# Kernel optimization log

Hardware: AMD Instinct MI355X
Metric: run time of the kernel (lower is better)

Reference implementation:

```python
import jax, jax.numpy as jnp
import numpy as np

TOP_K = 2

def setup_inputs() -> dict:
    key = jax.random.key(0)
    ks = jax.random.split(key, 7)
    B, L, D, H, E, S = 2, 2048, 1024, 512, 16, 2048
    s = lambda fan_in: (1.0 / np.sqrt(fan_in)).astype(np.float32)
    return {
        "x": jax.random.normal(ks[0], (B, L, D), jnp.float32),
        "gate_w": jax.random.normal(ks[1], (E, D), jnp.float32) * s(D),
        "w1": jax.random.normal(ks[2], (E, H, D), jnp.float32) * s(D),
        "w2": jax.random.normal(ks[3], (E, D, H), jnp.float32) * s(H),
        "sfc1": jax.random.normal(ks[4], (S, D), jnp.float32) * s(D),
        "sfc2": jax.random.normal(ks[5], (S, D), jnp.float32) * s(D),
        "sfc3": jax.random.normal(ks[6], (D, S), jnp.float32) * s(S),
    }

def reference(x, gate_w, w1, w2, sfc1, sfc2, sfc3):
    B, L, D = x.shape
    E = gate_w.shape[0]
    # shared expert: SwiGLU MLP
    shared = jnp.einsum("bls,ds->bld", jax.nn.silu(jnp.einsum("bld,sd->bls", x, sfc1)) * jnp.einsum("bld,sd->bls", x, sfc2), sfc3)
    # router: top-k over gate logits, softmax over selected logits only
    logits = jnp.einsum("bld,ed->ble", x, gate_w)
    top_w, top_idx = jax.lax.top_k(logits, TOP_K)           # [B,L,K]
    top_w = jax.nn.softmax(top_w, axis=-1)
    xf = x.reshape(-1, D)                                    # [T,D]
    T = xf.shape[0]
    idx = top_idx.reshape(T, TOP_K)
    wk = top_w.reshape(T, TOP_K)
    # dense combine weights [T,E]: routing weight where selected, else 0
    dispatch = jnp.zeros((T, E), xf.dtype).at[jnp.arange(T)[:, None], idx].add(wk)
    # all-expert dense compute, combined with dispatch weights (avoids [T,E,D])
    h = jax.nn.silu(jnp.einsum("td,ehd->teh", xf, w1))       # [T,E,H]
    moe = jnp.einsum("teh,te,edh->td", h, dispatch, w2)      # [T,D]
    return moe.reshape(B, L, D) + shared
```

## Files before the change

### kernel.cpp

```cpp
#include <hip/hip_runtime.h>
#include <stdint.h>

#define T_TOK 4096
#define D_DIM 1024
#define H_DIM 512
#define E_NUM 16
#define S_DIM 2048

#define DUAL_BLOCKS 512
#define MOE1_TILES_MAX 80
#define SHOUT_BLOCKS 256

typedef __attribute__((ext_vector_type(8))) __bf16 bf16x8;
typedef __attribute__((ext_vector_type(4))) float f32x4;

__device__ __forceinline__ uint16_t f2bf(float f) {
  uint32_t u = __float_as_uint(f);
  u += 0x7fffu + ((u >> 16) & 1u);
  return (uint16_t)(u >> 16);
}

__device__ __forceinline__ float bf2f(uint16_t u) {
  return __uint_as_float(((uint32_t)u) << 16);
}

__device__ __forceinline__ void gl_lds16(const void* g, void* l) {
  __builtin_amdgcn_global_load_lds(
      (const __attribute__((address_space(1))) void*)g,
      (__attribute__((address_space(3))) void*)l, 16, 0, 0);
}

__device__ __forceinline__ float silu_f(float v) {
  return v / (1.f + __expf(-v));
}

#define N4_X (T_TOK * D_DIM / 4)
#define N4_S (S_DIM * D_DIM / 4)
#define N4_W (E_NUM * H_DIM * D_DIM / 4)
#define N4_TOT (N4_X + 3 * N4_S + 2 * N4_W)

__global__ __launch_bounds__(256) void k_cast_all(
    const float* __restrict__ x, const float* __restrict__ sfc1,
    const float* __restrict__ sfc2, const float* __restrict__ sfc3,
    const float* __restrict__ w1, const float* __restrict__ w2,
    uint16_t* __restrict__ xb, uint16_t* __restrict__ s1b,
    uint16_t* __restrict__ s2b, uint16_t* __restrict__ s3b,
    uint16_t* __restrict__ w1b, uint16_t* __restrict__ w2b) {
  int i = blockIdx.x * 256 + threadIdx.x;
  if (i >= N4_TOT) return;
  const float* src; uint16_t* dst; int off;
  if (i < N4_X)                    { src = x;    dst = xb;  off = 0; }
  else if (i < N4_X + N4_S)        { src = sfc1; dst = s1b; off = N4_X; }
  else if (i < N4_X + 2 * N4_S)    { src = sfc2; dst = s2b; off = N4_X + N4_S; }
  else if (i < N4_X + 3 * N4_S)    { src = sfc3; dst = s3b; off = N4_X + 2 * N4_S; }
  else if (i < N4_X + 3 * N4_S + N4_W) { src = w1; dst = w1b; off = N4_X + 3 * N4_S; }
  else                             { src = w2;  dst = w2b; off = N4_X + 3 * N4_S + N4_W; }
  int j = i - off;
  float4 v = ((const float4*)src)[j];
  ushort4 o;
  o.x = f2bf(v.x); o.y = f2bf(v.y); o.z = f2bf(v.z); o.w = f2bf(v.w);
  ((ushort4*)dst)[j] = o;
}

__global__ void k_gwT(const float* __restrict__ gw, float4* __restrict__ gwT4) {
  int tid = blockIdx.x * 256 + threadIdx.x;
  if (tid >= E_NUM * (D_DIM / 4)) return;
  int k4 = tid & (D_DIM / 4 - 1);
  int e = tid >> 8;
  float4 v = ((const float4*)(gw + (size_t)e * D_DIM))[k4];
  gwT4[(size_t)k4 * E_NUM + e] = v;
}

__global__ __launch_bounds__(256) void k_router(
    const float* __restrict__ x, const float4* __restrict__ gwT4,
    int* __restrict__ top_idx, float* __restrict__ top_w) {
  const int wid = threadIdx.x >> 6, lane = threadIdx.x & 63;
  const int t = blockIdx.x * 4 + wid;
  const int e = lane & 15, q = lane >> 4;
  const float4* xr4 = (const float4*)(x + (size_t)t * D_DIM) + q * 64;
  const float4* g4 = gwT4 + (size_t)q * 64 * E_NUM + e;
  float acc = 0.f;
#pragma unroll 8
  for (int i = 0; i < 64; i++) {
    float4 xv = xr4[i];
    float4 gv = g4[(size_t)i * E_NUM];
    acc += xv.x * gv.x + xv.y * gv.y + xv.z * gv.z + xv.w * gv.w;
  }
  acc += __shfl_xor(acc, 16, 64);
  acc += __shfl_xor(acc, 32, 64);
  float v1 = acc; int i1 = e;
#pragma unroll
  for (int off = 1; off < 16; off <<= 1) {
    float ov = __shfl_xor(v1, off, 64);
    int oi = __shfl_xor(i1, off, 64);
    if (ov > v1 || (ov == v1 && oi < i1)) { v1 = ov; i1 = oi; }
  }
  float v2 = (e == i1) ? -1e30f : acc; int i2 = e;
#pragma unroll
  for (int off = 1; off < 16; off <<= 1) {
    float ov = __shfl_xor(v2, off, 64);
    int oi = __shfl_xor(i2, off, 64);
    if (ov > v2 || (ov == v2 && oi < i2)) { v2 = ov; i2 = oi; }
  }
  if (lane == 0) {
    float w0 = 1.f / (1.f + __expf(v2 - v1));
    top_idx[t * 2] = i1; top_idx[t * 2 + 1] = i2;
    top_w[t * 2] = w0;  top_w[t * 2 + 1] = 1.f - w0;
  }
}

__global__ __launch_bounds__(256) void k_hist(const int* __restrict__ top_idx,
                                              int* __restrict__ partial) {
  __shared__ int h[E_NUM];
  int tid = threadIdx.x;
  if (tid < E_NUM) h[tid] = 0;
  __syncthreads();
  int id = blockIdx.x * 256 + tid;
  atomicAdd(&h[top_idx[id]], 1);
  __syncthreads();
  if (tid < E_NUM) partial[blockIdx.x * E_NUM + tid] = h[tid];
}

__global__ void k_scan(const int* __restrict__ partial, int* __restrict__ bases,
                       int* __restrict__ offsets, int* __restrict__ tile_e,
                       int* __restrict__ tile_m, int* __restrict__ tile_cnt) {
  __shared__ int tot[E_NUM];
  int e = threadIdx.x;
  if (e < E_NUM) {
    int run = 0;
    for (int b = 0; b < 32; b++) { bases[b * E_NUM + e] = run; run += partial[b * E_NUM + e]; }
    tot[e] = run;
  }
  __syncthreads();
  if (e == 0) {
    int s = 0;
    for (int i = 0; i < E_NUM; i++) { offsets[i] = s; s += tot[i]; }
    offsets[E_NUM] = s;
    int cnt = 0;
    for (int i = 0; i < E_NUM; i++) {
      for (int m0 = 0; m0 < tot[i]; m0 += 128) {
        tile_e[cnt] = i; tile_m[cnt] = m0; cnt++;
      }
    }
    tile_cnt[0] = cnt;
  }
  __syncthreads();
  if (e < E_NUM) {
    int off = offsets[e];
    for (int b = 0; b < 32; b++) bases[b * E_NUM + e] += off;
  }
}

__global__ __launch_bounds__(256) void k_scatter(
    const int* __restrict__ top_idx, const float* __restrict__ top_w,
    const int* __restrict__ bases, int* __restrict__ slot_token,
    float* __restrict__ slot_w, int* __restrict__ slot_of) {
  __shared__ int cur[E_NUM];
  int tid = threadIdx.x;
  if (tid < E_NUM) cur[tid] = bases[blockIdx.x * E_NUM + tid];
  __syncthreads();
  int id = blockIdx.x * 256 + tid;
  int e = top_idx[id];
  int slot = atomicAdd(&cur[e], 1);
  slot_token[slot] = id >> 1;
  slot_w[slot] = top_w[id];
  slot_of[id] = slot;
}

__global__ __launch_bounds__(256) void k_stage1(
    const uint16_t* __restrict__ xb, const uint16_t* __restrict__ b1,
    const uint16_t* __restrict__ b2, uint16_t* __restrict__ hs,
    const uint16_t* __restrict__ w1b, const int* __restrict__ offsets,
    const int* __restrict__ slot_token, const int* __restrict__ tile_e,
    const int* __restrict__ tile_m, const int* __restrict__ tile_cnt,
    uint16_t* __restrict__ hbuf) {
  __shared__ uint16_t smem[3 * 4096];
  const int bid = blockIdx.x;
  const int tid = threadIdx.x, lane = tid & 63, wid = tid >> 6;
  const int wm = wid >> 1, wn = wid & 1;
  const int r = lane & 15, q = lane >> 4;
  const int row0 = tid >> 2, col8 = (tid & 3) * 8;

  if (bid < DUAL_BLOCKS) {
    const int bm0 = (bid & 31) * 128, bn0 = (bid >> 5) * 128;
    uint16_t* sA = smem; uint16_t* sB1 = smem + 4096; uint16_t* sB2 = smem + 8192;
    f32x4 acc1[4][4], acc2[4][4];
#pragma unroll
    for (int i = 0; i < 4; i++)
#pragma unroll
      for (int j = 0; j < 4; j++) {
        acc1[i][j] = (f32x4){0.f, 0.f, 0.f, 0.f};
        acc2[i][j] = (f32x4){0.f, 0.f, 0.f, 0.f};
      }
    const uint16_t* ga0 = xb + (size_t)(bm0 + row0) * D_DIM + col8;
    const uint16_t* ga1 = ga0 + 64 * D_DIM;
    const uint16_t* gb10 = b1 + (size_t)(bn0 + row0) * D_DIM + col8;
    const uint16_t* gb11 = gb10 + 64 * D_DIM;
    const uint16_t* gb20 = b2 + (size_t)(bn0 + row0) * D_DIM + col8;
    const uint16_t* gb21 = gb20 + 64 * D_DIM;
    for (int kt = 0; kt < D_DIM; kt += 32) {
      gl_lds16(ga0, sA + wid * 512);   gl_lds16(ga1, sA + 2048 + wid * 512);
      gl_lds16(gb10, sB1 + wid * 512); gl_lds16(gb11, sB1 + 2048 + wid * 512);
      gl_lds16(gb20, sB2 + wid * 512); gl_lds16(gb21, sB2 + 2048 + wid * 512);
      ga0 += 32; ga1 += 32; gb10 += 32; gb11 += 32; gb20 += 32; gb21 += 32;
      __syncthreads();
      bf16x8 a[4];
#pragma unroll
      for (int i = 0; i < 4; i++)
        a[i] = *(const bf16x8*)(sA + (wm * 64 + i * 16 + r) * 32 + q * 8);
#pragma unroll
      for (int j = 0; j < 4; j++) {
        bf16x8 b = *(const bf16x8*)(sB1 + (wn * 64 + j * 16 + r) * 32 + q * 8);
#pragma unroll
        for (int i = 0; i < 4; i++)
          acc1[i][j] = __builtin_amdgcn_mfma_f32_16x16x32_bf16(a[i], b, acc1[i][j], 0, 0, 0);
      }
#pragma unroll
      for (int j = 0; j < 4; j++) {
        bf16x8 b = *(const bf16x8*)(sB2 + (wn * 64 + j * 16 + r) * 32 + q * 8);
#pragma unroll
        for (int i = 0; i < 4; i++)
          acc2[i][j] = __builtin_amdgcn_mfma_f32_16x16x32_bf16(a[i], b, acc2[i][j], 0, 0, 0);
      }
      __syncthreads();
    }
#pragma unroll
    for (int i = 0; i < 4; i++)
#pragma unroll
      for (int j = 0; j < 4; j++)
#pragma unroll
        for (int rr = 0; rr < 4; rr++) {
          int row = bm0 + wm * 64 + i * 16 + q * 4 + rr;
          int col = bn0 + wn * 64 + j * 16 + r;
          hs[(size_t)row * S_DIM + col] = f2bf(silu_f(acc1[i][j][rr]) * acc2[i][j][rr]);
        }
  } else {
    int idx = bid - DUAL_BLOCKS;
    int t = idx >> 2;
    if (t >= tile_cnt[0]) return;
    const int n0 = (idx & 3) * 128;
    const int e = tile_e[t], m0 = tile_m[t];
    const int base = offsets[e];
    const int ne = offsets[e + 1] - base;
    uint16_t* sA = smem; uint16_t* sB = smem + 4096;
    f32x4 acc[4][4];
#pragma unroll
    for (int i = 0; i < 4; i++)
#pragma unroll
      for (int j = 0; j < 4; j++) acc[i][j] = (f32x4){0.f, 0.f, 0.f, 0.f};
    const int e0 = min(m0 + row0, ne - 1);
    const int e1 = min(m0 + row0 + 64, ne - 1);
    const uint16_t* ga0 = xb + (size_t)slot_token[base + e0] * D_DIM + col8;
    const uint16_t* ga1 = xb + (size_t)slot_token[base + e1] * D_DIM + col8;
    const uint16_t* wbase = w1b + (size_t)e * H_DIM * D_DIM;
    const uint16_t* gb0 = wbase + (size_t)(n0 + row0) * D_DIM + col8;
    const uint16_t* gb1 = gb0 + 64 * D_DIM;
    for (int kt = 0; kt < D_DIM; kt += 32) {
      gl_lds16(ga0, sA + wid * 512); gl_lds16(ga1, sA + 2048 + wid * 512);
      gl_lds16(gb0, sB + wid * 512); gl_lds16(gb1, sB + 2048 + wid * 512);
      ga0 += 32; ga1 += 32; gb0 += 32; gb1 += 32;
      __syncthreads();
      bf16x8 a[4], bb[4];
#pragma unroll
      for (int i = 0; i < 4; i++)
        a[i] = *(const bf16x8*)(sA + (wm * 64 + i * 16 + r) * 32 + q * 8);
#pragma unroll
      for (int j = 0; j < 4; j++)
        bb[j] = *(const bf16x8*)(sB + (wn * 64 + j * 16 + r) * 32 + q * 8);
#pragma unroll
      for (int i = 0; i < 4; i++)
#pragma unroll
        for (int j = 0; j < 4; j++)
          acc[i][j] = __builtin_amdgcn_mfma_f32_16x16x32_bf16(a[i], bb[j], acc[i][j], 0, 0, 0);
      __syncthreads();
    }
#pragma unroll
    for (int i = 0; i < 4; i++)
#pragma unroll
      for (int j = 0; j < 4; j++)
#pragma unroll
        for (int rr = 0; rr < 4; rr++) {
          int ent = m0 + wm * 64 + i * 16 + q * 4 + rr;
          if (ent < ne) {
            int col = n0 + wn * 64 + j * 16 + r;
            hbuf[(size_t)(base + ent) * H_DIM + col] = f2bf(silu_f(acc[i][j][rr]));
          }
        }
  }
}

__global__ __launch_bounds__(256) void k_stage2(
    const uint16_t* __restrict__ hsb, const uint16_t* __restrict__ sfc3b,
    float* __restrict__ out, const uint16_t* __restrict__ hbuf,
    const uint16_t* __restrict__ w2b, const int* __restrict__ offsets,
    const float* __restrict__ slot_w, const int* __restrict__ tile_e,
    const int* __restrict__ tile_m, const int* __restrict__ tile_cnt,
    uint16_t* __restrict__ slot_out) {
  __shared__ uint16_t smem[2 * 4096];
  const int bid = blockIdx.x;
  const int tid = threadIdx.x, lane = tid & 63, wid = tid >> 6;
  const int wm = wid >> 1, wn = wid & 1;
  const int r = lane & 15, q = lane >> 4;
  const int row0 = tid >> 2, col8 = (tid & 3) * 8;
  uint16_t* sA = smem; uint16_t* sB = smem + 4096;

  if (bid < SHOUT_BLOCKS) {
    const int bm0 = (bid & 31) * 128, bn0 = (bid >> 5) * 128;
    f32x4 acc[4][4];
#pragma unroll
    for (int i = 0; i < 4; i++)
#pragma unroll
      for (int j = 0; j < 4; j++) acc[i][j] = (f32x4){0.f, 0.f, 0.f, 0.f};
    const uint16_t* ga0 = hsb + (size_t)(bm0 + row0) * S_DIM + col8;
    const uint16_t* ga1 = ga0 + (size_t)64 * S_DIM;
    const uint16_t* gb0 = sfc3b + (size_t)(bn0 + row0) * S_DIM + col8;
    const uint16_t* gb1 = gb0 + (size_t)64 * S_DIM;
    for (int kt = 0; kt < S_DIM; kt += 32) {
      gl_lds16(ga0, sA + wid * 512); gl_lds16(ga1, sA + 2048 + wid * 512);
      gl_lds16(gb0, sB + wid * 512); gl_lds16(gb1, sB + 2048 + wid * 512);
      ga0 += 32; ga1 += 32; gb0 += 32; gb1 += 32;
      __syncthreads();
      bf16x8 a[4], bb[4];
#pragma unroll
      for (int i = 0; i < 4; i++)
        a[i] = *(const bf16x8*)(sA + (wm * 64 + i * 16 + r) * 32 + q * 8);
#pragma unroll
      for (int j = 0; j < 4; j++)
        bb[j] = *(const bf16x8*)(sB + (wn * 64 + j * 16 + r) * 32 + q * 8);
#pragma unroll
      for (int i = 0; i < 4; i++)
#pragma unroll
        for (int j = 0; j < 4; j++)
          acc[i][j] = __builtin_amdgcn_mfma_f32_16x16x32_bf16(a[i], bb[j], acc[i][j], 0, 0, 0);
      __syncthreads();
    }
#pragma unroll
    for (int i = 0; i < 4; i++)
#pragma unroll
      for (int j = 0; j < 4; j++)
#pragma unroll
        for (int rr = 0; rr < 4; rr++) {
          int row = bm0 + wm * 64 + i * 16 + q * 4 + rr;
          int col = bn0 + wn * 64 + j * 16 + r;
          out[(size_t)row * D_DIM + col] = acc[i][j][rr];
        }
  } else {
    int idx = bid - SHOUT_BLOCKS;
    int t = idx >> 3;
    if (t >= tile_cnt[0]) return;
    const int n0 = (idx & 7) * 128;
    const int e = tile_e[t], m0 = tile_m[t];
    const int base = offsets[e];
    const int ne = offsets[e + 1] - base;
    f32x4 acc[4][4];
#pragma unroll
    for (int i = 0; i < 4; i++)
#pragma unroll
      for (int j = 0; j < 4; j++) acc[i][j] = (f32x4){0.f, 0.f, 0.f, 0.f};
    const int e0 = min(m0 + row0, ne - 1);
    const int e1 = min(m0 + row0 + 64, ne - 1);
    const uint16_t* ga0 = hbuf + (size_t)(base + e0) * H_DIM + col8;
    const uint16_t* ga1 = hbuf + (size_t)(base + e1) * H_DIM + col8;
    const uint16_t* wbase = w2b + (size_t)e * D_DIM * H_DIM;
    const uint16_t* gb0 = wbase + (size_t)(n0 + row0) * H_DIM + col8;
    const uint16_t* gb1 = gb0 + 64 * H_DIM;
    for (int kt = 0; kt < H_DIM; kt += 32) {
      gl_lds16(ga0, sA + wid * 512); gl_lds16(ga1, sA + 2048 + wid * 512);
      gl_lds16(gb0, sB + wid * 512); gl_lds16(gb1, sB + 2048 + wid * 512);
      ga0 += 32; ga1 += 32; gb0 += 32; gb1 += 32;
      __syncthreads();
      bf16x8 a[4], bb[4];
#pragma unroll
      for (int i = 0; i < 4; i++)
        a[i] = *(const bf16x8*)(sA + (wm * 64 + i * 16 + r) * 32 + q * 8);
#pragma unroll
      for (int j = 0; j < 4; j++)
        bb[j] = *(const bf16x8*)(sB + (wn * 64 + j * 16 + r) * 32 + q * 8);
#pragma unroll
      for (int i = 0; i < 4; i++)
#pragma unroll
        for (int j = 0; j < 4; j++)
          acc[i][j] = __builtin_amdgcn_mfma_f32_16x16x32_bf16(a[i], bb[j], acc[i][j], 0, 0, 0);
      __syncthreads();
    }
#pragma unroll
    for (int i = 0; i < 4; i++) {
      int ent_base = m0 + wm * 64 + i * 16 + q * 4;
#pragma unroll
      for (int rr = 0; rr < 4; rr++) {
        int ent = ent_base + rr;
        if (ent < ne) {
          float w = slot_w[base + ent];
          uint16_t* orow = slot_out + (size_t)(base + ent) * D_DIM;
#pragma unroll
          for (int j = 0; j < 4; j++) {
            int col = n0 + wn * 64 + j * 16 + r;
            orow[col] = f2bf(w * acc[i][j][rr]);
          }
        }
      }
    }
  }
}

__global__ __launch_bounds__(256) void k_combine(
    const uint16_t* __restrict__ slot_out, const int* __restrict__ slot_of,
    float* __restrict__ out) {
  int t = blockIdx.x;
  int c = threadIdx.x;
  int s0 = slot_of[t * 2], s1 = slot_of[t * 2 + 1];
  ushort4 a = ((const ushort4*)(slot_out + (size_t)s0 * D_DIM))[c];
  ushort4 b = ((const ushort4*)(slot_out + (size_t)s1 * D_DIM))[c];
  float4* po = (float4*)(out + (size_t)t * D_DIM) + c;
  float4 o = *po;
  o.x += bf2f(a.x) + bf2f(b.x);
  o.y += bf2f(a.y) + bf2f(b.y);
  o.z += bf2f(a.z) + bf2f(b.z);
  o.w += bf2f(a.w) + bf2f(b.w);
  *po = o;
}

extern "C" void kernel_launch(void* const* d_in, const int* in_sizes, int n_in,
                              void* d_out, int out_size, void* d_ws, size_t ws_size,
                              hipStream_t stream) {
  const float* x     = (const float*)d_in[0];
  const float* gatew = (const float*)d_in[1];
  const float* w1    = (const float*)d_in[2];
  const float* w2    = (const float*)d_in[3];
  const float* sfc1  = (const float*)d_in[4];
  const float* sfc2  = (const float*)d_in[5];
  const float* sfc3  = (const float*)d_in[6];
  float* out = (float*)d_out;

  uint8_t* ws = (uint8_t*)d_ws;
  size_t off = 0;
  auto alloc = [&](size_t bytes) {
    void* p = ws + off;
    off = (off + bytes + 255) & ~(size_t)255;
    return p;
  };
  uint16_t* xb    = (uint16_t*)alloc((size_t)T_TOK * D_DIM * 2);
  uint16_t* sfc1b = (uint16_t*)alloc((size_t)S_DIM * D_DIM * 2);
  uint16_t* sfc2b = (uint16_t*)alloc((size_t)S_DIM * D_DIM * 2);
  uint16_t* sfc3b = (uint16_t*)alloc((size_t)D_DIM * S_DIM * 2);
  uint16_t* w1b   = (uint16_t*)alloc((size_t)E_NUM * H_DIM * D_DIM * 2);
  uint16_t* w2b   = (uint16_t*)alloc((size_t)E_NUM * D_DIM * H_DIM * 2);
  uint16_t* hsb   = (uint16_t*)alloc((size_t)T_TOK * S_DIM * 2);
  uint16_t* hbuf  = (uint16_t*)alloc((size_t)2 * T_TOK * H_DIM * 2);
  uint16_t* slot_out = (uint16_t*)alloc((size_t)2 * T_TOK * D_DIM * 2);
  float4* gwT4    = (float4*)alloc((size_t)D_DIM / 4 * E_NUM * 16);
  int*   top_idx  = (int*)alloc((size_t)T_TOK * 2 * 4);
  float* top_w    = (float*)alloc((size_t)T_TOK * 2 * 4);
  int*   partial  = (int*)alloc(32 * E_NUM * 4);
  int*   bases    = (int*)alloc(32 * E_NUM * 4);
  int*   offsets  = (int*)alloc((E_NUM + 1) * 4);
  int*   tile_e   = (int*)alloc(MOE1_TILES_MAX * 4);
  int*   tile_m   = (int*)alloc(MOE1_TILES_MAX * 4);
  int*   tile_cnt = (int*)alloc(4);
  int*   slot_token = (int*)alloc((size_t)2 * T_TOK * 4);
  float* slot_w   = (float*)alloc((size_t)2 * T_TOK * 4);
  int*   slot_of  = (int*)alloc((size_t)2 * T_TOK * 4);

  k_cast_all<<<(N4_TOT + 255) / 256, 256, 0, stream>>>(
      x, sfc1, sfc2, sfc3, w1, w2, xb, sfc1b, sfc2b, sfc3b, w1b, w2b);
  k_gwT<<<(E_NUM * D_DIM / 4 + 255) / 256, 256, 0, stream>>>(gatew, gwT4);
  k_router<<<T_TOK / 4, 256, 0, stream>>>(x, gwT4, top_idx, top_w);
  k_hist<<<32, 256, 0, stream>>>(top_idx, partial);
  k_scan<<<1, 64, 0, stream>>>(partial, bases, offsets, tile_e, tile_m, tile_cnt);
  k_scatter<<<32, 256, 0, stream>>>(top_idx, top_w, bases, slot_token, slot_w, slot_of);
  k_stage1<<<DUAL_BLOCKS + MOE1_TILES_MAX * 4, 256, 0, stream>>>(
      xb, sfc1b, sfc2b, hsb, w1b, offsets, slot_token, tile_e, tile_m, tile_cnt, hbuf);
  k_stage2<<<SHOUT_BLOCKS + MOE1_TILES_MAX * 8, 256, 0, stream>>>(
      hsb, sfc3b, out, hbuf, w2b, offsets, slot_w, tile_e, tile_m, tile_cnt, slot_out);
  k_combine<<<T_TOK, 256, 0, stream>>>(slot_out, slot_of, out);
}
```

Baseline: 349.5 us.

## Double-buffer LDS tiles with register prefetch in all GEMM loops

Replaces direct global-to-LDS loads with register-staged loads into a double-buffered LDS tile. The next K-slice is fetched into registers while the current slice's MFMAs run, then stored to the alternate buffer, leaving one barrier per iteration instead of two. This aims to hide global load latency behind compute. The cost is double the LDS footprint and extra VGPRs for the staged data, which may reduce occupancy.

```diff
diff --git a/kernel.cpp b/kernel.cpp
--- a/kernel.cpp
+++ b/kernel.cpp
@@ -22,12 +22,6 @@
 
 __device__ __forceinline__ float bf2f(uint16_t u) {
   return __uint_as_float(((uint32_t)u) << 16);
-}
-
-__device__ __forceinline__ void gl_lds16(const void* g, void* l) {
-  __builtin_amdgcn_global_load_lds(
-      (const __attribute__((address_space(1))) void*)g,
-      (__attribute__((address_space(3))) void*)l, 16, 0, 0);
 }
 
 __device__ __forceinline__ float silu_f(float v) {
@@ -167,6 +161,7 @@
   slot_of[id] = slot;
 }
 
+
 __global__ __launch_bounds__(256) void k_stage1(
     const uint16_t* __restrict__ xb, const uint16_t* __restrict__ b1,
     const uint16_t* __restrict__ b2, uint16_t* __restrict__ hs,
@@ -174,16 +169,19 @@
     const int* __restrict__ slot_token, const int* __restrict__ tile_e,
     const int* __restrict__ tile_m, const int* __restrict__ tile_cnt,
     uint16_t* __restrict__ hbuf) {
-  __shared__ uint16_t smem[3 * 4096];
+  __shared__ uint16_t smem[6 * 4096];
   const int bid = blockIdx.x;
   const int tid = threadIdx.x, lane = tid & 63, wid = tid >> 6;
   const int wm = wid >> 1, wn = wid & 1;
   const int r = lane & 15, q = lane >> 4;
   const int row0 = tid >> 2, col8 = (tid & 3) * 8;
+  const int st0 = tid * 8, st1 = 2048 + tid * 8;
 
   if (bid < DUAL_BLOCKS) {
     const int bm0 = (bid & 31) * 128, bn0 = (bid >> 5) * 128;
-    uint16_t* sA = smem; uint16_t* sB1 = smem + 4096; uint16_t* sB2 = smem + 8192;
+    uint16_t* sA = smem;
+    uint16_t* sB1 = smem + 8192;
+    uint16_t* sB2 = smem + 16384;
     f32x4 acc1[4][4], acc2[4][4];
 #pragma unroll
     for (int i = 0; i < 4; i++)
@@ -198,31 +196,75 @@
     const uint16_t* gb11 = gb10 + 64 * D_DIM;
     const uint16_t* gb20 = b2 + (size_t)(bn0 + row0) * D_DIM + col8;
     const uint16_t* gb21 = gb20 + 64 * D_DIM;
-    for (int kt = 0; kt < D_DIM; kt += 32) {
-      gl_lds16(ga0, sA + wid * 512);   gl_lds16(ga1, sA + 2048 + wid * 512);
-      gl_lds16(gb10, sB1 + wid * 512); gl_lds16(gb11, sB1 + 2048 + wid * 512);
-      gl_lds16(gb20, sB2 + wid * 512); gl_lds16(gb21, sB2 + 2048 + wid * 512);
+
+    uint4 pA0, pA1, pB10, pB11, pB20, pB21;
+    pA0 = *(const uint4*)ga0;   pA1 = *(const uint4*)ga1;
+    pB10 = *(const uint4*)gb10; pB11 = *(const uint4*)gb11;
+    pB20 = *(const uint4*)gb20; pB21 = *(const uint4*)gb21;
+    ga0 += 32; ga1 += 32; gb10 += 32; gb11 += 32; gb20 += 32; gb21 += 32;
+    *(uint4*)(sA + st0) = pA0;   *(uint4*)(sA + st1) = pA1;
+    *(uint4*)(sB1 + st0) = pB10; *(uint4*)(sB1 + st1) = pB11;
+    *(uint4*)(sB2 + st0) = pB20; *(uint4*)(sB2 + st1) = pB21;
+    __syncthreads();
+
+    int cur = 0;
+    for (int kt = 32; kt < D_DIM; kt += 32) {
+      pA0 = *(const uint4*)ga0;   pA1 = *(const uint4*)ga1;
+      pB10 = *(const uint4*)gb10; pB11 = *(const uint4*)gb11;
+      pB20 = *(const uint4*)gb20; pB21 = *(const uint4*)gb21;
       ga0 += 32; ga1 += 32; gb10 += 32; gb11 += 32; gb20 += 32; gb21 += 32;
+      {
+        const uint16_t* A = sA + cur * 4096;
+        const uint16_t* B1 = sB1 + cur * 4096;
+        const uint16_t* B2 = sB2 + cur * 4096;
+        bf16x8 a[4];
+#pragma unroll
+        for (int i = 0; i < 4; i++)
+          a[i] = *(const bf16x8*)(A + (wm * 64 + i * 16 + r) * 32 + q * 8);
+#pragma unroll
+        for (int j = 0; j < 4; j++) {
+          bf16x8 b = *(const bf16x8*)(B1 + (wn * 64 + j * 16 + r) * 32 + q * 8);
+#pragma unroll
+          for (int i = 0; i < 4; i++)
+            acc1[i][j] = __builtin_amdgcn_mfma_f32_16x16x32_bf16(a[i], b, acc1[i][j], 0, 0, 0);
+        }
+#pragma unroll
+        for (int j = 0; j < 4; j++) {
+          bf16x8 b = *(const bf16x8*)(B2 + (wn * 64 + j * 16 + r) * 32 + q * 8);
+#pragma unroll
+          for (int i = 0; i < 4; i++)
+            acc2[i][j] = __builtin_amdgcn_mfma_f32_16x16x32_bf16(a[i], b, acc2[i][j], 0, 0, 0);
+        }
+      }
+      int nxt = cur ^ 1;
+      *(uint4*)(sA + nxt * 4096 + st0) = pA0;   *(uint4*)(sA + nxt * 4096 + st1) = pA1;
+      *(uint4*)(sB1 + nxt * 4096 + st0) = pB10; *(uint4*)(sB1 + nxt * 4096 + st1) = pB11;
+      *(uint4*)(sB2 + nxt * 4096 + st0) = pB20; *(uint4*)(sB2 + nxt * 4096 + st1) = pB21;
       __syncthreads();
+      cur = nxt;
+    }
+    {
+      const uint16_t* A = sA + cur * 4096;
+      const uint16_t* B1 = sB1 + cur * 4096;
+      const uint16_t* B2 = sB2 + cur * 4096;
       bf16x8 a[4];
 #pragma unroll
       for (int i = 0; i < 4; i++)
-        a[i] = *(const bf16x8*)(sA + (wm * 64 + i * 16 + r) * 32 + q * 8);
+        a[i] = *(const bf16x8*)(A + (wm * 64 + i * 16 + r) * 32 + q * 8);
 #pragma unroll
       for (int j = 0; j < 4; j++) {
-        bf16x8 b = *(const bf16x8*)(sB1 + (wn * 64 + j * 16 + r) * 32 + q * 8);
+        bf16x8 b = *(const bf16x8*)(B1 + (wn * 64 + j * 16 + r) * 32 + q * 8);
 #pragma unroll
         for (int i = 0; i < 4; i++)
           acc1[i][j] = __builtin_amdgcn_mfma_f32_16x16x32_bf16(a[i], b, acc1[i][j], 0, 0, 0);
       }
 #pragma unroll
       for (int j = 0; j < 4; j++) {
-        bf16x8 b = *(const bf16x8*)(sB2 + (wn * 64 + j * 16 + r) * 32 + q * 8);
+        bf16x8 b = *(const bf16x8*)(B2 + (wn * 64 + j * 16 + r) * 32 + q * 8);
 #pragma unroll
         for (int i = 0; i < 4; i++)
           acc2[i][j] = __builtin_amdgcn_mfma_f32_16x16x32_bf16(a[i], b, acc2[i][j], 0, 0, 0);
       }
-      __syncthreads();
     }
 #pragma unroll
     for (int i = 0; i < 4; i++)
@@ -242,7 +284,8 @@
     const int e = tile_e[t], m0 = tile_m[t];
     const int base = offsets[e];
     const int ne = offsets[e + 1] - base;
-    uint16_t* sA = smem; uint16_t* sB = smem + 4096;
+    uint16_t* sA = smem;
+    uint16_t* sB = smem + 8192;
     f32x4 acc[4][4];
 #pragma unroll
     for (int i = 0; i < 4; i++)
@@ -255,24 +298,57 @@
     const uint16_t* wbase = w1b + (size_t)e * H_DIM * D_DIM;
     const uint16_t* gb0 = wbase + (size_t)(n0 + row0) * D_DIM + col8;
     const uint16_t* gb1 = gb0 + 64 * D_DIM;
-    for (int kt = 0; kt < D_DIM; kt += 32) {
-      gl_lds16(ga0, sA + wid * 512); gl_lds16(ga1, sA + 2048 + wid * 512);
-      gl_lds16(gb0, sB + wid * 512); gl_lds16(gb1, sB + 2048 + wid * 512);
+
+    uint4 pA0, pA1, pB0, pB1;
+    pA0 = *(const uint4*)ga0; pA1 = *(const uint4*)ga1;
+    pB0 = *(const uint4*)gb0; pB1 = *(const uint4*)gb1;
+    ga0 += 32; ga1 += 32; gb0 += 32; gb1 += 32;
+    *(uint4*)(sA + st0) = pA0; *(uint4*)(sA + st1) = pA1;
+    *(uint4*)(sB + st0) = pB0; *(uint4*)(sB + st1) = pB1;
+    __syncthreads();
+
+    int cur = 0;
+    for (int kt = 32; kt < D_DIM; kt += 32) {
+      pA0 = *(const uint4*)ga0; pA1 = *(const uint4*)ga1;
+      pB0 = *(const uint4*)gb0; pB1 = *(const uint4*)gb1;
       ga0 += 32; ga1 += 32; gb0 += 32; gb1 += 32;
+      {
+        const uint16_t* A = sA + cur * 4096;
+        const uint16_t* B = sB + cur * 4096;
+        bf16x8 a[4], bb[4];
+#pragma unroll
+        for (int i = 0; i < 4; i++)
+          a[i] = *(const bf16x8*)(A + (wm * 64 + i * 16 + r) * 32 + q * 8);
+#pragma unroll
+        for (int j = 0; j < 4; j++)
+          bb[j] = *(const bf16x8*)(B + (wn * 64 + j * 16 + r) * 32 + q * 8);
+#pragma unroll
+        for (int i = 0; i < 4; i++)
+#pragma unroll
+          for (int j = 0; j < 4; j++)
+            acc[i][j] = __builtin_amdgcn_mfma_f32_16x16x32_bf16(a[i], bb[j], acc[i][j], 0, 0, 0);
+      }
+      int nxt = cur ^ 1;
+      *(uint4*)(sA + nxt * 4096 + st0) = pA0; *(uint4*)(sA + nxt * 4096 + st1) = pA1;
+      *(uint4*)(sB + nxt * 4096 + st0) = pB0; *(uint4*)(sB + nxt * 4096 + st1) = pB1;
       __syncthreads();
+      cur = nxt;
+    }
+    {
+      const uint16_t* A = sA + cur * 4096;
+      const uint16_t* B = sB + cur * 4096;
       bf16x8 a[4], bb[4];
 #pragma unroll
       for (int i = 0; i < 4; i++)
-        a[i] = *(const bf16x8*)(sA + (wm * 64 + i * 16 + r) * 32 + q * 8);
+        a[i] = *(const bf16x8*)(A + (wm * 64 + i * 16 + r) * 32 + q * 8);
 #pragma unroll
       for (int j = 0; j < 4; j++)
-        bb[j] = *(const bf16x8*)(sB + (wn * 64 + j * 16 + r) * 32 + q * 8);
+        bb[j] = *(const bf16x8*)(B + (wn * 64 + j * 16 + r) * 32 + q * 8);
 #pragma unroll
       for (int i = 0; i < 4; i++)
 #pragma unroll
         for (int j = 0; j < 4; j++)
           acc[i][j] = __builtin_amdgcn_mfma_f32_16x16x32_bf16(a[i], bb[j], acc[i][j], 0, 0, 0);
-      __syncthreads();
     }
 #pragma unroll
     for (int i = 0; i < 4; i++)
@@ -296,13 +372,15 @@
     const float* __restrict__ slot_w, const int* __restrict__ tile_e,
     const int* __restrict__ tile_m, const int* __restrict__ tile_cnt,
     uint16_t* __restrict__ slot_out) {
-  __shared__ uint16_t smem[2 * 4096];
+  __shared__ uint16_t smem[4 * 4096];
   const int bid = blockIdx.x;
   const int tid = threadIdx.x, lane = tid & 63, wid = tid >> 6;
   const int wm = wid >> 1, wn = wid & 1;
   const int r = lane & 15, q = lane >> 4;
   const int row0 = tid >> 2, col8 = (tid & 3) * 8;
-  uint16_t* sA = smem; uint16_t* sB = smem + 4096;
+  const int st0 = tid * 8, st1 = 2048 + tid * 8;
+  uint16_t* sA = smem;
+  uint16_t* sB = smem + 8192;
 
   if (bid < SHOUT_BLOCKS) {
     const int bm0 = (bid & 31) * 128, bn0 = (bid >> 5) * 128;
@@ -315,24 +393,57 @@
     const uint16_t* ga1 = ga0 + (size_t)64 * S_DIM;
     const uint16_t* gb0 = sfc3b + (size_t)(bn0 + row0) * S_DIM + col8;
     const uint16_t* gb1 = gb0 + (size_t)64 * S_DIM;
-    for (int kt = 0; kt < S_DIM; kt += 32) {
-      gl_lds16(ga0, sA + wid * 512); gl_lds16(ga1, sA + 2048 + wid * 512);
-      gl_lds16(gb0, sB + wid * 512); gl_lds16(gb1, sB + 2048 + wid * 512);
+
+    uint4 pA0, pA1, pB0, pB1;
+    pA0 = *(const uint4*)ga0; pA1 = *(const uint4*)ga1;
+    pB0 = *(const uint4*)gb0; pB1 = *(const uint4*)gb1;
+    ga0 += 32; ga1 += 32; gb0 += 32; gb1 += 32;
+    *(uint4*)(sA + st0) = pA0; *(uint4*)(sA + st1) = pA1;
+    *(uint4*)(sB + st0) = pB0; *(uint4*)(sB + st1) = pB1;
+    __syncthreads();
+
+    int cur = 0;
+    for (int kt = 32; kt < S_DIM; kt += 32) {
+      pA0 = *(const uint4*)ga0; pA1 = *(const uint4*)ga1;
+      pB0 = *(const uint4*)gb0; pB1 = *(const uint4*)gb1;
       ga0 += 32; ga1 += 32; gb0 += 32; gb1 += 32;
+      {
+        const uint16_t* A = sA + cur * 4096;
+        const uint16_t* B = sB + cur * 4096;
+        bf16x8 a[4], bb[4];
+#pragma unroll
+        for (int i = 0; i < 4; i++)
+          a[i] = *(const bf16x8*)(A + (wm * 64 + i * 16 + r) * 32 + q * 8);
+#pragma unroll
+        for (int j = 0; j < 4; j++)
+          bb[j] = *(const bf16x8*)(B + (wn * 64 + j * 16 + r) * 32 + q * 8);
+#pragma unroll
+        for (int i = 0; i < 4; i++)
+#pragma unroll
+          for (int j = 0; j < 4; j++)
+            acc[i][j] = __builtin_amdgcn_mfma_f32_16x16x32_bf16(a[i], bb[j], acc[i][j], 0, 0, 0);
+      }
+      int nxt = cur ^ 1;
+      *(uint4*)(sA + nxt * 4096 + st0) = pA0; *(uint4*)(sA + nxt * 4096 + st1) = pA1;
+      *(uint4*)(sB + nxt * 4096 + st0) = pB0; *(uint4*)(sB + nxt * 4096 + st1) = pB1;
       __syncthreads();
+      cur = nxt;
+    }
+    {
+      const uint16_t* A = sA + cur * 4096;
+      const uint16_t* B = sB + cur * 4096;
       bf16x8 a[4], bb[4];
 #pragma unroll
       for (int i = 0; i < 4; i++)
-        a[i] = *(const bf16x8*)(sA + (wm * 64 + i * 16 + r) * 32 + q * 8);
+        a[i] = *(const bf16x8*)(A + (wm * 64 + i * 16 + r) * 32 + q * 8);
 #pragma unroll
       for (int j = 0; j < 4; j++)
-        bb[j] = *(const bf16x8*)(sB + (wn * 64 + j * 16 + r) * 32 + q * 8);
+        bb[j] = *(const bf16x8*)(B + (wn * 64 + j * 16 + r) * 32 + q * 8);
 #pragma unroll
       for (int i = 0; i < 4; i++)
 #pragma unroll
         for (int j = 0; j < 4; j++)
           acc[i][j] = __builtin_amdgcn_mfma_f32_16x16x32_bf16(a[i], bb[j], acc[i][j], 0, 0, 0);
-      __syncthreads();
     }
 #pragma unroll
     for (int i = 0; i < 4; i++)
@@ -364,24 +475,57 @@
     const uint16_t* wbase = w2b + (size_t)e * D_DIM * H_DIM;
     const uint16_t* gb0 = wbase + (size_t)(n0 + row0) * H_DIM + col8;
     const uint16_t* gb1 = gb0 + 64 * H_DIM;
-    for (int kt = 0; kt < H_DIM; kt += 32) {
-      gl_lds16(ga0, sA + wid * 512); gl_lds16(ga1, sA + 2048 + wid * 512);
-      gl_lds16(gb0, sB + wid * 512); gl_lds16(gb1, sB + 2048 + wid * 512);
+
+    uint4 pA0, pA1, pB0, pB1;
+    pA0 = *(const uint4*)ga0; pA1 = *(const uint4*)ga1;
+    pB0 = *(const uint4*)gb0; pB1 = *(const uint4*)gb1;
+    ga0 += 32; ga1 += 32; gb0 += 32; gb1 += 32;
+    *(uint4*)(sA + st0) = pA0; *(uint4*)(sA + st1) = pA1;
+    *(uint4*)(sB + st0) = pB0; *(uint4*)(sB + st1) = pB1;
+    __syncthreads();
+
+    int cur = 0;
+    for (int kt = 32; kt < H_DIM; kt += 32) {
+      pA0 = *(const uint4*)ga0; pA1 = *(const uint4*)ga1;
+      pB0 = *(const uint4*)gb0; pB1 = *(const uint4*)gb1;
       ga0 += 32; ga1 += 32; gb0 += 32; gb1 += 32;
+      {
+        const uint16_t* A = sA + cur * 4096;
+        const uint16_t* B = sB + cur * 4096;
+        bf16x8 a[4], bb[4];
+#pragma unroll
+        for (int i = 0; i < 4; i++)
+          a[i] = *(const bf16x8*)(A + (wm * 64 + i * 16 + r) * 32 + q * 8);
+#pragma unroll
+        for (int j = 0; j < 4; j++)
+          bb[j] = *(const bf16x8*)(B + (wn * 64 + j * 16 + r) * 32 + q * 8);
+#pragma unroll
+        for (int i = 0; i < 4; i++)
+#pragma unroll
+          for (int j = 0; j < 4; j++)
+            acc[i][j] = __builtin_amdgcn_mfma_f32_16x16x32_bf16(a[i], bb[j], acc[i][j], 0, 0, 0);
+      }
+      int nxt = cur ^ 1;
+      *(uint4*)(sA + nxt * 4096 + st0) = pA0; *(uint4*)(sA + nxt * 4096 + st1) = pA1;
+      *(uint4*)(sB + nxt * 4096 + st0) = pB0; *(uint4*)(sB + nxt * 4096 + st1) = pB1;
       __syncthreads();
+      cur = nxt;
+    }
+    {
+      const uint16_t* A = sA + cur * 4096;
+      const uint16_t* B = sB + cur * 4096;
       bf16x8 a[4], bb[4];
 #pragma unroll
       for (int i = 0; i < 4; i++)
-        a[i] = *(const bf16x8*)(sA + (wm * 64 + i * 16 + r) * 32 + q * 8);
+        a[i] = *(const bf16x8*)(A + (wm * 64 + i * 16 + r) * 32 + q * 8);
 #pragma unroll
       for (int j = 0; j < 4; j++)
-        bb[j] = *(const bf16x8*)(sB + (wn * 64 + j * 16 + r) * 32 + q * 8);
+        bb[j] = *(const bf16x8*)(B + (wn * 64 + j * 16 + r) * 32 + q * 8);
 #pragma unroll
       for (int i = 0; i < 4; i++)
 #pragma unroll
         for (int j = 0; j < 4; j++)
           acc[i][j] = __builtin_amdgcn_mfma_f32_16x16x32_bf16(a[i], bb[j], acc[i][j], 0, 0, 0);
-      __syncthreads();
     }
 #pragma unroll
     for (int i = 0; i < 4; i++) {
```

After: 306.0 us. 12.4% less time.

## Double-buffer GEMM tiles via register prefetch and split shared SwiGLU into separate GEMMs

Applied to the files above, without the earlier changes.

Replaces the direct global-to-LDS loads with a shared double-buffered GEMM loop that prefetches the next K tile into registers while MFMAs run on the current LDS buffer. This halves the barriers per step and overlaps load latency with compute. The dual-accumulator shared-expert GEMM is split into two single-B GEMMs, giving twice as many blocks with lower register pressure. Their bf16 outputs go to new buffers, and a separate silu-multiply kernel combines them. This adds extra global traffic (two 16MB intermediates written and read) and an extra launch, and rounds the gate products to bf16 before the SiLU.

```diff
diff --git a/kernel.cpp b/kernel.cpp
--- a/kernel.cpp
+++ b/kernel.cpp
@@ -7,7 +7,7 @@
 #define E_NUM 16
 #define S_DIM 2048
 
-#define DUAL_BLOCKS 512
+#define G_BLOCKS 512
 #define MOE1_TILES_MAX 80
 #define SHOUT_BLOCKS 256
 
@@ -22,12 +22,6 @@
 
 __device__ __forceinline__ float bf2f(uint16_t u) {
   return __uint_as_float(((uint32_t)u) << 16);
-}
-
-__device__ __forceinline__ void gl_lds16(const void* g, void* l) {
-  __builtin_amdgcn_global_load_lds(
-      (const __attribute__((address_space(1))) void*)g,
-      (__attribute__((address_space(3))) void*)l, 16, 0, 0);
 }
 
 __device__ __forceinline__ float silu_f(float v) {
@@ -137,11 +131,8 @@
     for (int i = 0; i < E_NUM; i++) { offsets[i] = s; s += tot[i]; }
     offsets[E_NUM] = s;
     int cnt = 0;
-    for (int i = 0; i < E_NUM; i++) {
-      for (int m0 = 0; m0 < tot[i]; m0 += 128) {
-        tile_e[cnt] = i; tile_m[cnt] = m0; cnt++;
-      }
-    }
+    for (int i = 0; i < E_NUM; i++)
+      for (int m0 = 0; m0 < tot[i]; m0 += 128) { tile_e[cnt] = i; tile_m[cnt] = m0; cnt++; }
     tile_cnt[0] = cnt;
   }
   __syncthreads();
@@ -167,63 +158,101 @@
   slot_of[id] = slot;
 }
 
+__device__ __forceinline__ void gemm128_loop(
+    const uint16_t* ga0, const uint16_t* ga1,
+    const uint16_t* gb0, const uint16_t* gb1,
+    uint16_t* sA, uint16_t* sB, int kiters, int tid,
+    f32x4 (&acc)[4][4]) {
+  const int lane = tid & 63, wid = tid >> 6;
+  const int wm = wid >> 1, wn = wid & 1;
+  const int r = lane & 15, q = lane >> 4;
+  const int st0 = tid * 8, st1 = 2048 + tid * 8;
+
+  uint4 pA0 = *(const uint4*)ga0, pA1 = *(const uint4*)ga1;
+  uint4 pB0 = *(const uint4*)gb0, pB1 = *(const uint4*)gb1;
+  ga0 += 32; ga1 += 32; gb0 += 32; gb1 += 32;
+  *(uint4*)(sA + st0) = pA0; *(uint4*)(sA + st1) = pA1;
+  *(uint4*)(sB + st0) = pB0; *(uint4*)(sB + st1) = pB1;
+  __syncthreads();
+
+  int cur = 0;
+  for (int kt = 1; kt < kiters; kt++) {
+    pA0 = *(const uint4*)ga0; pA1 = *(const uint4*)ga1;
+    pB0 = *(const uint4*)gb0; pB1 = *(const uint4*)gb1;
+    ga0 += 32; ga1 += 32; gb0 += 32; gb1 += 32;
+    {
+      const uint16_t* A = sA + cur * 4096;
+      const uint16_t* B = sB + cur * 4096;
+      bf16x8 a[4], bb[4];
+#pragma unroll
+      for (int i = 0; i < 4; i++)
+        a[i] = *(const bf16x8*)(A + (wm * 64 + i * 16 + r) * 32 + q * 8);
+#pragma unroll
+      for (int j = 0; j < 4; j++)
+        bb[j] = *(const bf16x8*)(B + (wn * 64 + j * 16 + r) * 32 + q * 8);
+#pragma unroll
+      for (int i = 0; i < 4; i++)
+#pragma unroll
+        for (int j = 0; j < 4; j++)
+          acc[i][j] = __builtin_amdgcn_mfma_f32_16x16x32_bf16(a[i], bb[j], acc[i][j], 0, 0, 0);
+    }
+    int nxt = cur ^ 1;
+    *(uint4*)(sA + nxt * 4096 + st0) = pA0; *(uint4*)(sA + nxt * 4096 + st1) = pA1;
+    *(uint4*)(sB + nxt * 4096 + st0) = pB0; *(uint4*)(sB + nxt * 4096 + st1) = pB1;
+    __syncthreads();
+    cur = nxt;
+  }
+  {
+    const uint16_t* A = sA + cur * 4096;
+    const uint16_t* B = sB + cur * 4096;
+    bf16x8 a[4], bb[4];
+#pragma unroll
+    for (int i = 0; i < 4; i++)
+      a[i] = *(const bf16x8*)(A + (wm * 64 + i * 16 + r) * 32 + q * 8);
+#pragma unroll
+    for (int j = 0; j < 4; j++)
+      bb[j] = *(const bf16x8*)(B + (wn * 64 + j * 16 + r) * 32 + q * 8);
+#pragma unroll
+    for (int i = 0; i < 4; i++)
+#pragma unroll
+      for (int j = 0; j < 4; j++)
+        acc[i][j] = __builtin_amdgcn_mfma_f32_16x16x32_bf16(a[i], bb[j], acc[i][j], 0, 0, 0);
+  }
+}
+
 __global__ __launch_bounds__(256) void k_stage1(
     const uint16_t* __restrict__ xb, const uint16_t* __restrict__ b1,
-    const uint16_t* __restrict__ b2, uint16_t* __restrict__ hs,
-    const uint16_t* __restrict__ w1b, const int* __restrict__ offsets,
-    const int* __restrict__ slot_token, const int* __restrict__ tile_e,
-    const int* __restrict__ tile_m, const int* __restrict__ tile_cnt,
-    uint16_t* __restrict__ hbuf) {
-  __shared__ uint16_t smem[3 * 4096];
+    const uint16_t* __restrict__ b2, uint16_t* __restrict__ g1,
+    uint16_t* __restrict__ g2, const uint16_t* __restrict__ w1b,
+    const int* __restrict__ offsets, const int* __restrict__ slot_token,
+    const int* __restrict__ tile_e, const int* __restrict__ tile_m,
+    const int* __restrict__ tile_cnt, uint16_t* __restrict__ hbuf) {
+  __shared__ uint16_t smem[4 * 4096];
+  uint16_t* sA = smem;
+  uint16_t* sB = smem + 8192;
   const int bid = blockIdx.x;
   const int tid = threadIdx.x, lane = tid & 63, wid = tid >> 6;
   const int wm = wid >> 1, wn = wid & 1;
   const int r = lane & 15, q = lane >> 4;
   const int row0 = tid >> 2, col8 = (tid & 3) * 8;
 
-  if (bid < DUAL_BLOCKS) {
-    const int bm0 = (bid & 31) * 128, bn0 = (bid >> 5) * 128;
-    uint16_t* sA = smem; uint16_t* sB1 = smem + 4096; uint16_t* sB2 = smem + 8192;
-    f32x4 acc1[4][4], acc2[4][4];
-#pragma unroll
-    for (int i = 0; i < 4; i++)
-#pragma unroll
-      for (int j = 0; j < 4; j++) {
-        acc1[i][j] = (f32x4){0.f, 0.f, 0.f, 0.f};
-        acc2[i][j] = (f32x4){0.f, 0.f, 0.f, 0.f};
-      }
+  f32x4 acc[4][4];
+#pragma unroll
+  for (int i = 0; i < 4; i++)
+#pragma unroll
+    for (int j = 0; j < 4; j++) acc[i][j] = (f32x4){0.f, 0.f, 0.f, 0.f};
+
+  if (bid < 2 * G_BLOCKS) {
+    const int gi = (bid >= G_BLOCKS);
+    const int idx = gi ? bid - G_BLOCKS : bid;
+    const int bm0 = (idx & 31) * 128, bn0 = (idx >> 5) * 128;
+    const uint16_t* bmat = gi ? b2 : b1;
+    uint16_t* gout = gi ? g2 : g1;
     const uint16_t* ga0 = xb + (size_t)(bm0 + row0) * D_DIM + col8;
     const uint16_t* ga1 = ga0 + 64 * D_DIM;
-    const uint16_t* gb10 = b1 + (size_t)(bn0 + row0) * D_DIM + col8;
-    const uint16_t* gb11 = gb10 + 64 * D_DIM;
-    const uint16_t* gb20 = b2 + (size_t)(bn0 + row0) * D_DIM + col8;
-    const uint16_t* gb21 = gb20 + 64 * D_DIM;
-    for (int kt = 0; kt < D_DIM; kt += 32) {
-      gl_lds16(ga0, sA + wid * 512);   gl_lds16(ga1, sA + 2048 + wid * 512);
-      gl_lds16(gb10, sB1 + wid * 512); gl_lds16(gb11, sB1 + 2048 + wid * 512);
-      gl_lds16(gb20, sB2 + wid * 512); gl_lds16(gb21, sB2 + 2048 + wid * 512);
-      ga0 += 32; ga1 += 32; gb10 += 32; gb11 += 32; gb20 += 32; gb21 += 32;
-      __syncthreads();
-      bf16x8 a[4];
-#pragma unroll
-      for (int i = 0; i < 4; i++)
-        a[i] = *(const bf16x8*)(sA + (wm * 64 + i * 16 + r) * 32 + q * 8);
-#pragma unroll
-      for (int j = 0; j < 4; j++) {
-        bf16x8 b = *(const bf16x8*)(sB1 + (wn * 64 + j * 16 + r) * 32 + q * 8);
-#pragma unroll
-        for (int i = 0; i < 4; i++)
-          acc1[i][j] = __builtin_amdgcn_mfma_f32_16x16x32_bf16(a[i], b, acc1[i][j], 0, 0, 0);
-      }
-#pragma unroll
-      for (int j = 0; j < 4; j++) {
-        bf16x8 b = *(const bf16x8*)(sB2 + (wn * 64 + j * 16 + r) * 32 + q * 8);
-#pragma unroll
-        for (int i = 0; i < 4; i++)
-          acc2[i][j] = __builtin_amdgcn_mfma_f32_16x16x32_bf16(a[i], b, acc2[i][j], 0, 0, 0);
-      }
-      __syncthreads();
-    }
+    const uint16_t* gb0 = bmat + (size_t)(bn0 + row0) * D_DIM + col8;
+    const uint16_t* gb1 = gb0 + 64 * D_DIM;
+    gemm128_loop(ga0, ga1, gb0, gb1, sA, sB, D_DIM / 32, tid, acc);
 #pragma unroll
     for (int i = 0; i < 4; i++)
 #pragma unroll
@@ -232,22 +261,16 @@
         for (int rr = 0; rr < 4; rr++) {
           int row = bm0 + wm * 64 + i * 16 + q * 4 + rr;
           int col = bn0 + wn * 64 + j * 16 + r;
-          hs[(size_t)row * S_DIM + col] = f2bf(silu_f(acc1[i][j][rr]) * acc2[i][j][rr]);
+          gout[(size_t)row * S_DIM + col] = f2bf(acc[i][j][rr]);
         }
   } else {
-    int idx = bid - DUAL_BLOCKS;
+    int idx = bid - 2 * G_BLOCKS;
     int t = idx >> 2;
     if (t >= tile_cnt[0]) return;
     const int n0 = (idx & 3) * 128;
     const int e = tile_e[t], m0 = tile_m[t];
     const int base = offsets[e];
     const int ne = offsets[e + 1] - base;
-    uint16_t* sA = smem; uint16_t* sB = smem + 4096;
-    f32x4 acc[4][4];
-#pragma unroll
-    for (int i = 0; i < 4; i++)
-#pragma unroll
-      for (int j = 0; j < 4; j++) acc[i][j] = (f32x4){0.f, 0.f, 0.f, 0.f};
     const int e0 = min(m0 + row0, ne - 1);
     const int e1 = min(m0 + row0 + 64, ne - 1);
     const uint16_t* ga0 = xb + (size_t)slot_token[base + e0] * D_DIM + col8;
@@ -255,25 +278,7 @@
     const uint16_t* wbase = w1b + (size_t)e * H_DIM * D_DIM;
     const uint16_t* gb0 = wbase + (size_t)(n0 + row0) * D_DIM + col8;
     const uint16_t* gb1 = gb0 + 64 * D_DIM;
-    for (int kt = 0; kt < D_DIM; kt += 32) {
-      gl_lds16(ga0, sA + wid * 512); gl_lds16(ga1, sA + 2048 + wid * 512);
-      gl_lds16(gb0, sB + wid * 512); gl_lds16(gb1, sB + 2048 + wid * 512);
-      ga0 += 32; ga1 += 32; gb0 += 32; gb1 += 32;
-      __syncthreads();
-      bf16x8 a[4], bb[4];
-#pragma unroll
-      for (int i = 0; i < 4; i++)
-        a[i] = *(const bf16x8*)(sA + (wm * 64 + i * 16 + r) * 32 + q * 8);
-#pragma unroll
-      for (int j = 0; j < 4; j++)
-        bb[j] = *(const bf16x8*)(sB + (wn * 64 + j * 16 + r) * 32 + q * 8);
-#pragma unroll
-      for (int i = 0; i < 4; i++)
-#pragma unroll
-        for (int j = 0; j < 4; j++)
-          acc[i][j] = __builtin_amdgcn_mfma_f32_16x16x32_bf16(a[i], bb[j], acc[i][j], 0, 0, 0);
-      __syncthreads();
-    }
+    gemm128_loop(ga0, ga1, gb0, gb1, sA, sB, D_DIM / 32, tid, acc);
 #pragma unroll
     for (int i = 0; i < 4; i++)
 #pragma unroll
@@ -289,6 +294,21 @@
   }
 }
 
+__global__ __launch_bounds__(256) void k_silumul(
+    const uint16_t* __restrict__ g1, const uint16_t* __restrict__ g2,
+    uint16_t* __restrict__ hs) {
+  int i = blockIdx.x * 256 + threadIdx.x;
+  uint4 a = ((const uint4*)g1)[i];
+  uint4 b = ((const uint4*)g2)[i];
+  const uint16_t* pa = (const uint16_t*)&a;
+  const uint16_t* pb = (const uint16_t*)&b;
+  uint4 o;
+  uint16_t* po = (uint16_t*)&o;
+#pragma unroll
+  for (int k = 0; k < 8; k++) po[k] = f2bf(silu_f(bf2f(pa[k])) * bf2f(pb[k]));
+  ((uint4*)hs)[i] = o;
+}
+
 __global__ __launch_bounds__(256) void k_stage2(
     const uint16_t* __restrict__ hsb, const uint16_t* __restrict__ sfc3b,
     float* __restrict__ out, const uint16_t* __restrict__ hbuf,
@@ -296,44 +316,28 @@
     const float* __restrict__ slot_w, const int* __restrict__ tile_e,
     const int* __restrict__ tile_m, const int* __restrict__ tile_cnt,
     uint16_t* __restrict__ slot_out) {
-  __shared__ uint16_t smem[2 * 4096];
+  __shared__ uint16_t smem[4 * 4096];
+  uint16_t* sA = smem;
+  uint16_t* sB = smem + 8192;
   const int bid = blockIdx.x;
   const int tid = threadIdx.x, lane = tid & 63, wid = tid >> 6;
   const int wm = wid >> 1, wn = wid & 1;
   const int r = lane & 15, q = lane >> 4;
   const int row0 = tid >> 2, col8 = (tid & 3) * 8;
-  uint16_t* sA = smem; uint16_t* sB = smem + 4096;
+
+  f32x4 acc[4][4];
+#pragma unroll
+  for (int i = 0; i < 4; i++)
+#pragma unroll
+    for (int j = 0; j < 4; j++) acc[i][j] = (f32x4){0.f, 0.f, 0.f, 0.f};
 
   if (bid < SHOUT_BLOCKS) {
     const int bm0 = (bid & 31) * 128, bn0 = (bid >> 5) * 128;
-    f32x4 acc[4][4];
-#pragma unroll
-    for (int i = 0; i < 4; i++)
-#pragma unroll
-      for (int j = 0; j < 4; j++) acc[i][j] = (f32x4){0.f, 0.f, 0.f, 0.f};
     const uint16_t* ga0 = hsb + (size_t)(bm0 + row0) * S_DIM + col8;
     const uint16_t* ga1 = ga0 + (size_t)64 * S_DIM;
     const uint16_t* gb0 = sfc3b + (size_t)(bn0 + row0) * S_DIM + col8;
     const uint16_t* gb1 = gb0 + (size_t)64 * S_DIM;
-    for (int kt = 0; kt < S_DIM; kt += 32) {
-      gl_lds16(ga0, sA + wid * 512); gl_lds16(ga1, sA + 2048 + wid * 512);
-      gl_lds16(gb0, sB + wid * 512); gl_lds16(gb1, sB + 2048 + wid * 512);
-      ga0 += 32; ga1 += 32; gb0 += 32; gb1 += 32;
-      __syncthreads();
-      bf16x8 a[4], bb[4];
-#pragma unroll
-      for (int i = 0; i < 4; i++)
-        a[i] = *(const bf16x8*)(sA + (wm * 64 + i * 16 + r) * 32 + q * 8);
-#pragma unroll
-      for (int j = 0; j < 4; j++)
-        bb[j] = *(const bf16x8*)(sB + (wn * 64 + j * 16 + r) * 32 + q * 8);
-#pragma unroll
-      for (int i = 0; i < 4; i++)
-#pragma unroll
-        for (int j = 0; j < 4; j++)
-          acc[i][j] = __builtin_amdgcn_mfma_f32_16x16x32_bf16(a[i], bb[j], acc[i][j], 0, 0, 0);
-      __syncthreads();
-    }
+    gemm128_loop(ga0, ga1, gb0, gb1, sA, sB, S_DIM / 32, tid, acc);
 #pragma unroll
     for (int i = 0; i < 4; i++)
 #pragma unroll
@@ -352,11 +356,6 @@
     const int e = tile_e[t], m0 = tile_m[t];
     const int base = offsets[e];
     const int ne = offsets[e + 1] - base;
-    f32x4 acc[4][4];
-#pragma unroll
-    for (int i = 0; i < 4; i++)
-#pragma unroll
-      for (int j = 0; j < 4; j++) acc[i][j] = (f32x4){0.f, 0.f, 0.f, 0.f};
     const int e0 = min(m0 + row0, ne - 1);
     const int e1 = min(m0 + row0 + 64, ne - 1);
     const uint16_t* ga0 = hbuf + (size_t)(base + e0) * H_DIM + col8;
@@ -364,25 +363,7 @@
     const uint16_t* wbase = w2b + (size_t)e * D_DIM * H_DIM;
     const uint16_t* gb0 = wbase + (size_t)(n0 + row0) * H_DIM + col8;
     const uint16_t* gb1 = gb0 + 64 * H_DIM;
-    for (int kt = 0; kt < H_DIM; kt += 32) {
-      gl_lds16(ga0, sA + wid * 512); gl_lds16(ga1, sA + 2048 + wid * 512);
-      gl_lds16(gb0, sB + wid * 512); gl_lds16(gb1, sB + 2048 + wid * 512);
-      ga0 += 32; ga1 += 32; gb0 += 32; gb1 += 32;
-      __syncthreads();
-      bf16x8 a[4], bb[4];
-#pragma unroll
-      for (int i = 0; i < 4; i++)
-        a[i] = *(const bf16x8*)(sA + (wm * 64 + i * 16 + r) * 32 + q * 8);
-#pragma unroll
-      for (int j = 0; j < 4; j++)
-        bb[j] = *(const bf16x8*)(sB + (wn * 64 + j * 16 + r) * 32 + q * 8);
-#pragma unroll
-      for (int i = 0; i < 4; i++)
-#pragma unroll
-        for (int j = 0; j < 4; j++)
-          acc[i][j] = __builtin_amdgcn_mfma_f32_16x16x32_bf16(a[i], bb[j], acc[i][j], 0, 0, 0);
-      __syncthreads();
-    }
+    gemm128_loop(ga0, ga1, gb0, gb1, sA, sB, H_DIM / 32, tid, acc);
 #pragma unroll
     for (int i = 0; i < 4; i++) {
       int ent_base = m0 + wm * 64 + i * 16 + q * 4;
@@ -445,6 +426,8 @@
   uint16_t* sfc3b = (uint16_t*)alloc((size_t)D_DIM * S_DIM * 2);
   uint16_t* w1b   = (uint16_t*)alloc((size_t)E_NUM * H_DIM * D_DIM * 2);
   uint16_t* w2b   = (uint16_t*)alloc((size_t)E_NUM * D_DIM * H_DIM * 2);
+  uint16_t* g1buf = (uint16_t*)alloc((size_t)T_TOK * S_DIM * 2);
+  uint16_t* g2buf = (uint16_t*)alloc((size_t)T_TOK * S_DIM * 2);
   uint16_t* hsb   = (uint16_t*)alloc((size_t)T_TOK * S_DIM * 2);
   uint16_t* hbuf  = (uint16_t*)alloc((size_t)2 * T_TOK * H_DIM * 2);
   uint16_t* slot_out = (uint16_t*)alloc((size_t)2 * T_TOK * D_DIM * 2);
@@ -468,8 +451,10 @@
   k_hist<<<32, 256, 0, stream>>>(top_idx, partial);
   k_scan<<<1, 64, 0, stream>>>(partial, bases, offsets, tile_e, tile_m, tile_cnt);
   k_scatter<<<32, 256, 0, stream>>>(top_idx, top_w, bases, slot_token, slot_w, slot_of);
-  k_stage1<<<DUAL_BLOCKS + MOE1_TILES_MAX * 4, 256, 0, stream>>>(
-      xb, sfc1b, sfc2b, hsb, w1b, offsets, slot_token, tile_e, tile_m, tile_cnt, hbuf);
+  k_stage1<<<2 * G_BLOCKS + MOE1_TILES_MAX * 4, 256, 0, stream>>>(
+      xb, sfc1b, sfc2b, g1buf, g2buf, w1b, offsets, slot_token,
+      tile_e, tile_m, tile_cnt, hbuf);
+  k_silumul<<<T_TOK * S_DIM / 8 / 256, 256, 0, stream>>>(g1buf, g2buf, hsb);
   k_stage2<<<SHOUT_BLOCKS + MOE1_TILES_MAX * 8, 256, 0, stream>>>(
       hsb, sfc3b, out, hbuf, w2b, offsets, slot_w, tile_e, tile_m, tile_cnt, slot_out);
   k_combine<<<T_TOK, 256, 0, stream>>>(slot_out, slot_of, out);
```

Result: faster. 318.4 us (-8.9%).
